# Performance work log

Measured on AMD Instinct MI355X. Metric: run time of the kernel, lower is better.

The kernel has to match this reference:

```python
import jax, jax.numpy as jnp
import numpy as np

B, N, D = 32, 2048, 16
PCD = 2        # point_cloud_dimensions
K_NN = 16      # k nearest neighbours
FILTERS = 64


def setup_inputs() -> dict:
    key = jax.random.key(0)
    k1, k2, k3 = jax.random.split(key, 3)
    x = jax.random.normal(k1, (B, N, D), dtype=jnp.float32)
    # 1x1 Conv2D == dense over the last (channel) dim: W [D, FILTERS], b [FILTERS]
    W = jax.random.normal(k2, (D, FILTERS), dtype=jnp.float32) * (1.0 / np.sqrt(D))
    b = jnp.zeros((FILTERS,), dtype=jnp.float32)
    return {"x": x, "W": W, "b": b}


def reference(x, W, b):
    # points = first PCD channels; features = full input (dynamic_coordinates=True)
    points = x[:, :, :PCD]                                   # [B,N,PCD]
    # squared pairwise distances: ||p_i||^2 + ||p_j||^2 - 2 p_i.p_j  -> [B,N,N]
    sq = jnp.sum(points * points, axis=-1)                   # [B,N]
    dist = sq[:, :, None] + sq[:, None, :] - 2.0 * jnp.einsum(
        'bnd,bmd->bnm', points, points)
    # k nearest neighbours (smallest distance) per point -> [B,N,k]
    _, idx = jax.lax.top_k(-dist, K_NN)
    # gather neighbour features: [B,N,k,D]
    neigh = jax.vmap(lambda f, i: f[i])(x, idx)
    centre = x[:, :, None, :]                                # [B,N,1,D]
    # NOTE: source concatenates along the neighbour axis -> [B,N,k+1,D]
    edges = jnp.concatenate([centre, neigh - centre], axis=2)
    # 1x1 conv (linear activation) over channel dim: [B,N,k+1,FILTERS]
    conv = jnp.einsum('bnkd,df->bnkf', edges, W) + b
    # Max pooling over neighbour axis: [B,N,FILTERS]
    pooled = jnp.max(conv, axis=2)
    # shortcut_input_features=True: concat original features
    return jnp.concatenate([pooled, x], axis=-1)             # [B,N,FILTERS+D]
```

## Files before the change

kernel.cpp:

```cpp
#include <hip/hip_runtime.h>


#define B_  32
#define N_  2048
#define D_  16
#define F_  64
#define K_  16
#define OUTD (F_ + D_)
#define NQ  64
#define NS  4
#define SPLIT (N_ / NS)

__global__ __launch_bounds__(256) void proj_kernel(const float* __restrict__ x,
                                                   const float* __restrict__ W,
                                                   float* __restrict__ Y) {
    __shared__ float Ws[D_ * F_];
    __shared__ float xs[16][D_];
    const int t = threadIdx.x;
    for (int i = t; i < D_ * F_; i += 256) Ws[i] = W[i];
    const int p0 = blockIdx.x * 16;
    ((float*)xs)[t] = x[(size_t)p0 * D_ + t];
    __syncthreads();
    const int w = t >> 6, f = t & 63;
#pragma unroll
    for (int i = 0; i < 4; i++) {
        const int pw = w * 4 + i;
        float acc = 0.f;
#pragma unroll
        for (int d = 0; d < D_; d++) acc = fmaf(xs[pw][d], Ws[d * F_ + f], acc);
        Y[(size_t)(p0 + pw) * F_ + f] = acc;
    }
}

__global__ __launch_bounds__(256, 4) void knn_kernel(const float* __restrict__ x,
                                                     const float* __restrict__ bias,
                                                     const float* __restrict__ Y,
                                                     float* __restrict__ out) {
    __shared__ float2 pts[N_];
    __shared__ float  sqs[N_];
    __shared__ float  arr_raw[NS - 1][NQ * 17];
    __shared__ float  Tq[NQ];
    __shared__ int    cnt[NQ];
    __shared__ int    tiecnt[NS][NQ];
    unsigned short (*tiebuf)[NQ][K_] =
        (unsigned short (*)[NQ][K_])&arr_raw[0][0];
    int (*idxL)[K_] = (int (*)[K_])((char*)&arr_raw[0][0] + 8192);

    const int b = blockIdx.x >> 5;
    const int qbase = (blockIdx.x & 31) * NQ;
    const int t = threadIdx.x;
    const int s = t >> 6;
    const int qi = t & 63;
    const int q = qbase + qi;

    const float* xb = x + (size_t)b * N_ * D_;
    for (int m = t; m < N_; m += 256) {
        float2 p = make_float2(xb[m * D_ + 0], xb[m * D_ + 1]);
        pts[m] = p;
        sqs[m] = __fadd_rn(__fmul_rn(p.x, p.x), __fmul_rn(p.y, p.y));
    }
    if (t < NQ) cnt[t] = 0;
    __syncthreads();

    const float2 qp = pts[q];
    const float sqn = sqs[q];

    float key[K_];
#pragma unroll
    for (int j = 0; j < K_; j++) key[j] = INFINITY;

    const int m0 = s * SPLIT, m1 = m0 + SPLIT;
#pragma unroll 4
    for (int m = m0; m < m1; m += 2) {
        float2 pa = pts[m];     float sa = sqs[m];
        float2 pb = pts[m + 1]; float sb = sqs[m + 1];
        float dota = __fmaf_rn(qp.y, pa.y, __fmul_rn(qp.x, pa.x));
        float da   = __fsub_rn(__fadd_rn(sqn, sa), __fmul_rn(2.f, dota));
        float dotb = __fmaf_rn(qp.y, pb.y, __fmul_rn(qp.x, pb.x));
        float db   = __fsub_rn(__fadd_rn(sqn, sb), __fmul_rn(2.f, dotb));
        float y0 = fminf(da, db), y1 = fmaxf(da, db);
#pragma unroll
        for (int j = K_ - 1; j >= 2; j--)
            key[j] = fminf(fminf(key[j], fmaxf(key[j - 1], y0)),
                           fmaxf(key[j - 2], y1));
        key[1] = fminf(fminf(key[1], fmaxf(key[0], y0)), y1);
        key[0] = fminf(key[0], y0);
    }

    if (s > 0) {
#pragma unroll
        for (int j = 0; j < K_; j++) arr_raw[s - 1][qi * 17 + j] = key[j];
    }
    __syncthreads();

    if (s == 0) {
        for (int ss = 0; ss < NS - 1; ss++) {
#pragma unroll
            for (int j = 0; j < K_; j += 2) {
                float y0 = arr_raw[ss][qi * 17 + j];
                float y1 = arr_raw[ss][qi * 17 + j + 1];
#pragma unroll
                for (int jj = K_ - 1; jj >= 2; jj--)
                    key[jj] = fminf(fminf(key[jj], fmaxf(key[jj - 1], y0)),
                                    fmaxf(key[jj - 2], y1));
                key[1] = fminf(fminf(key[1], fmaxf(key[0], y0)), y1);
                key[0] = fminf(key[0], y0);
            }
        }
        Tq[qi] = key[K_ - 1];
    }
    __syncthreads();

    const float T = Tq[qi];
    int tc = 0;
#pragma unroll 2
    for (int m = m0; m < m1; m++) {
        float2 p = pts[m];
        float dot = __fmaf_rn(qp.y, p.y, __fmul_rn(qp.x, p.x));
        float d   = __fsub_rn(__fadd_rn(sqn, sqs[m]), __fmul_rn(2.f, dot));
        if (d < T) {
            int slot = atomicAdd(&cnt[qi], 1);
            idxL[qi][slot] = m;
        } else if (d == T) {
            if (tc < K_) tiebuf[s][qi][tc] = (unsigned short)m;
            tc++;
        }
    }
    tiecnt[s][qi] = (tc < K_) ? tc : K_;
    __syncthreads();

    if (s == 0) {
        int c1 = cnt[qi];
        int w = c1;
        int need = K_ - c1;
        for (int ss = 0; ss < NS && need > 0; ss++) {
            int nn = tiecnt[ss][qi];
            for (int j = 0; j < nn && need > 0; j++) {
                idxL[qi][w++] = (int)tiebuf[ss][qi][j];
                need--;
            }
        }
    }
    __syncthreads();

    const int f = qi;
    const float bf = bias[f];
    const float* Yb = Y + (size_t)b * N_ * F_;
    for (int i = 0; i < 16; i++) {
        const int qq = s * 16 + i;
        const int gq = qbase + qq;
        const float yn = Yb[(size_t)gq * F_ + f];
        float M = -INFINITY;
#pragma unroll
        for (int k = 0; k < K_; k++) {
            int m = idxL[qq][k];
            M = fmaxf(M, Yb[(size_t)m * F_ + f]);
        }
        const size_t pb = (size_t)b * N_ + gq;
        out[pb * OUTD + f] = fmaxf(yn, M - yn) + bf;
        if (f < D_) out[pb * OUTD + F_ + f] = xb[(size_t)gq * D_ + f];
    }
}

extern "C" void kernel_launch(void* const* d_in, const int* in_sizes, int n_in,
                              void* d_out, int out_size, void* d_ws, size_t ws_size,
                              hipStream_t stream) {
    const float* x    = (const float*)d_in[0];
    const float* W    = (const float*)d_in[1];
    const float* bias = (const float*)d_in[2];
    float* out = (float*)d_out;

    float* Y = (float*)d_ws;

    proj_kernel<<<B_ * N_ / 16, 256, 0, stream>>>(x, W, Y);
    knn_kernel <<<B_ * (N_ / NQ), 256, 0, stream>>>(x, bias, Y, out);
}
```

Measured before the change: 259.4 us.

## Sort points by x and prune kNN scans with early termination

Adds a per-batch bitonic sort of points by their x coordinate, then has each query scan outward in both directions along the sorted order. A scan stops once the squared x-gap exceeds the current k-th distance plus a margin. This replaces the brute-force scan over all N points with a small local window. Tie handling is reworked to keep original-index order, so results should match the reference. The cost is an extra sort kernel with many block-level syncs, divergent per-thread loop lengths, and lower occupancy because of the added shared arrays.

Result: slower. 481.0 us (+85.5%).

```diff
diff --git a/kernel.cpp b/kernel.cpp
--- a/kernel.cpp
+++ b/kernel.cpp
@@ -9,17 +9,56 @@
 #define OUTD (F_ + D_)
 #define NQ  64
 #define NS  4
-#define SPLIT (N_ / NS)
+#define MARGIN 1e-3f
+
+__global__ __launch_bounds__(256) void sort_kernel(const float* __restrict__ x,
+                                                   float* __restrict__ xs,
+                                                   float* __restrict__ ys,
+                                                   unsigned short* __restrict__ oidx) {
+    __shared__ float keyL[N_];
+    __shared__ int   valL[N_];
+    const int bidx = blockIdx.x;
+    const int t = threadIdx.x;
+    const float* xb = x + (size_t)bidx * N_ * D_;
+    for (int m = t; m < N_; m += 256) { keyL[m] = xb[(size_t)m * D_]; valL[m] = m; }
+    for (int k = 2; k <= N_; k <<= 1) {
+        for (int j = k >> 1; j > 0; j >>= 1) {
+            __syncthreads();
+            for (int i = t; i < N_; i += 256) {
+                int ixj = i ^ j;
+                if (ixj > i) {
+                    float a = keyL[i], c = keyL[ixj];
+                    bool up = ((i & k) == 0);
+                    bool sw = up ? (a > c) : (a < c);
+                    if (sw) {
+                        keyL[i] = c; keyL[ixj] = a;
+                        int tv = valL[i]; valL[i] = valL[ixj]; valL[ixj] = tv;
+                    }
+                }
+            }
+        }
+    }
+    __syncthreads();
+    float* xso = xs + (size_t)bidx * N_;
+    float* yso = ys + (size_t)bidx * N_;
+    unsigned short* oio = oidx + (size_t)bidx * N_;
+    for (int p = t; p < N_; p += 256) {
+        int v = valL[p];
+        xso[p] = keyL[p];
+        yso[p] = xb[(size_t)v * D_ + 1];
+        oio[p] = (unsigned short)v;
+    }
+}
 
 __global__ __launch_bounds__(256) void proj_kernel(const float* __restrict__ x,
                                                    const float* __restrict__ W,
                                                    float* __restrict__ Y) {
     __shared__ float Ws[D_ * F_];
-    __shared__ float xs[16][D_];
+    __shared__ float xsh[16][D_];
     const int t = threadIdx.x;
     for (int i = t; i < D_ * F_; i += 256) Ws[i] = W[i];
     const int p0 = blockIdx.x * 16;
-    ((float*)xs)[t] = x[(size_t)p0 * D_ + t];
+    ((float*)xsh)[t] = x[(size_t)p0 * D_ + t];
     __syncthreads();
     const int w = t >> 6, f = t & 63;
 #pragma unroll
@@ -27,17 +66,22 @@
         const int pw = w * 4 + i;
         float acc = 0.f;
 #pragma unroll
-        for (int d = 0; d < D_; d++) acc = fmaf(xs[pw][d], Ws[d * F_ + f], acc);
+        for (int d = 0; d < D_; d++) acc = fmaf(xsh[pw][d], Ws[d * F_ + f], acc);
         Y[(size_t)(p0 + pw) * F_ + f] = acc;
     }
 }
 
-__global__ __launch_bounds__(256, 4) void knn_kernel(const float* __restrict__ x,
+__global__ __launch_bounds__(256, 3) void knn_kernel(const float* __restrict__ x,
                                                      const float* __restrict__ bias,
                                                      const float* __restrict__ Y,
+                                                     const float* __restrict__ xs,
+                                                     const float* __restrict__ ys,
+                                                     const unsigned short* __restrict__ oidx,
                                                      float* __restrict__ out) {
-    __shared__ float2 pts[N_];
-    __shared__ float  sqs[N_];
+    __shared__ float  xsL[N_];
+    __shared__ float  ysL[N_];
+    __shared__ float  sqL[N_];
+    __shared__ unsigned short oiL[N_];
     __shared__ float  arr_raw[NS - 1][NQ * 17];
     __shared__ float  Tq[NQ];
     __shared__ int    cnt[NQ];
@@ -53,31 +97,44 @@
     const int qi = t & 63;
     const int q = qbase + qi;
 
-    const float* xb = x + (size_t)b * N_ * D_;
+    const float* xsb = xs + (size_t)b * N_;
+    const float* ysb = ys + (size_t)b * N_;
+    const unsigned short* oib = oidx + (size_t)b * N_;
     for (int m = t; m < N_; m += 256) {
-        float2 p = make_float2(xb[m * D_ + 0], xb[m * D_ + 1]);
-        pts[m] = p;
-        sqs[m] = __fadd_rn(__fmul_rn(p.x, p.x), __fmul_rn(p.y, p.y));
+        float xv = xsb[m];
+        float yv = ysb[m];
+        xsL[m] = xv;
+        ysL[m] = yv;
+        sqL[m] = __fadd_rn(__fmul_rn(xv, xv), __fmul_rn(yv, yv));
+        oiL[m] = oib[m];
     }
     if (t < NQ) cnt[t] = 0;
     __syncthreads();
 
-    const float2 qp = pts[q];
-    const float sqn = sqs[q];
+    const float qx = xsL[q];
+    const float qy = ysL[q];
+    const float sqn = sqL[q];
+
+    const int pstart = q + ((s == 0) ? 0 : (s == 1) ? 1 : (s == 2) ? -1 : -2);
+    const int pstep  = (s < 2) ? 2 : -2;
 
     float key[K_];
 #pragma unroll
     for (int j = 0; j < K_; j++) key[j] = INFINITY;
 
-    const int m0 = s * SPLIT, m1 = m0 + SPLIT;
-#pragma unroll 4
-    for (int m = m0; m < m1; m += 2) {
-        float2 pa = pts[m];     float sa = sqs[m];
-        float2 pb = pts[m + 1]; float sb = sqs[m + 1];
-        float dota = __fmaf_rn(qp.y, pa.y, __fmul_rn(qp.x, pa.x));
-        float da   = __fsub_rn(__fadd_rn(sqn, sa), __fmul_rn(2.f, dota));
-        float dotb = __fmaf_rn(qp.y, pb.y, __fmul_rn(qp.x, pb.x));
-        float db   = __fsub_rn(__fadd_rn(sqn, sb), __fmul_rn(2.f, dotb));
+    for (int p = pstart; (unsigned)p < (unsigned)N_; p += 2 * pstep) {
+        float xma = xsL[p];
+        float dxa = xma - qx;
+        if (dxa * dxa > key[K_ - 1] + MARGIN) break;
+        float dota = __fmaf_rn(qy, ysL[p], __fmul_rn(qx, xma));
+        float da   = __fsub_rn(__fadd_rn(sqn, sqL[p]), __fmul_rn(2.f, dota));
+        float db = INFINITY;
+        const int p2 = p + pstep;
+        if ((unsigned)p2 < (unsigned)N_) {
+            float xmb = xsL[p2];
+            float dotb = __fmaf_rn(qy, ysL[p2], __fmul_rn(qx, xmb));
+            db = __fsub_rn(__fadd_rn(sqn, sqL[p2]), __fmul_rn(2.f, dotb));
+        }
         float y0 = fminf(da, db), y1 = fmaxf(da, db);
 #pragma unroll
         for (int j = K_ - 1; j >= 2; j--)
@@ -113,16 +170,23 @@
 
     const float T = Tq[qi];
     int tc = 0;
-#pragma unroll 2
-    for (int m = m0; m < m1; m++) {
-        float2 p = pts[m];
-        float dot = __fmaf_rn(qp.y, p.y, __fmul_rn(qp.x, p.x));
-        float d   = __fsub_rn(__fadd_rn(sqn, sqs[m]), __fmul_rn(2.f, dot));
+    for (int p = pstart; (unsigned)p < (unsigned)N_; p += pstep) {
+        float xm = xsL[p];
+        float dx = xm - qx;
+        if (dx * dx > T + MARGIN) break;
+        float dot = __fmaf_rn(qy, ysL[p], __fmul_rn(qx, xm));
+        float d   = __fsub_rn(__fadd_rn(sqn, sqL[p]), __fmul_rn(2.f, dot));
         if (d < T) {
             int slot = atomicAdd(&cnt[qi], 1);
-            idxL[qi][slot] = m;
+            idxL[qi][slot] = (int)oiL[p];
         } else if (d == T) {
-            if (tc < K_) tiebuf[s][qi][tc] = (unsigned short)m;
+            int oi = (int)oiL[p];
+            int pos = (tc < K_) ? tc : K_;
+            while (pos > 0 && (int)tiebuf[s][qi][pos - 1] > oi) {
+                if (pos < K_) tiebuf[s][qi][pos] = tiebuf[s][qi][pos - 1];
+                pos--;
+            }
+            if (pos < K_) tiebuf[s][qi][pos] = (unsigned short)oi;
             tc++;
         }
     }
@@ -131,14 +195,22 @@
 
     if (s == 0) {
         int c1 = cnt[qi];
-        int w = c1;
-        int need = K_ - c1;
-        for (int ss = 0; ss < NS && need > 0; ss++) {
-            int nn = tiecnt[ss][qi];
-            for (int j = 0; j < nn && need > 0; j++) {
-                idxL[qi][w++] = (int)tiebuf[ss][qi][j];
-                need--;
-            }
+        int l0 = tiecnt[0][qi], l1 = tiecnt[1][qi];
+        int l2 = tiecnt[2][qi], l3 = tiecnt[3][qi];
+        int p0 = 0, p1 = 0, p2 = 0, p3 = 0;
+        for (int w = c1; w < K_; w++) {
+            int v0 = (p0 < l0) ? (int)tiebuf[0][qi][p0] : 0x7fffffff;
+            int v1 = (p1 < l1) ? (int)tiebuf[1][qi][p1] : 0x7fffffff;
+            int v2 = (p2 < l2) ? (int)tiebuf[2][qi][p2] : 0x7fffffff;
+            int v3 = (p3 < l3) ? (int)tiebuf[3][qi][p3] : 0x7fffffff;
+            int m01 = (v0 <= v1) ? v0 : v1;
+            int m23 = (v2 <= v3) ? v2 : v3;
+            int mv  = (m01 <= m23) ? m01 : m23;
+            idxL[qi][w] = mv;
+            if (mv == v0) p0++;
+            else if (mv == v1) p1++;
+            else if (mv == v2) p2++;
+            else p3++;
         }
     }
     __syncthreads();
@@ -146,19 +218,20 @@
     const int f = qi;
     const float bf = bias[f];
     const float* Yb = Y + (size_t)b * N_ * F_;
+    const float* xb = x + (size_t)b * N_ * D_;
     for (int i = 0; i < 16; i++) {
         const int qq = s * 16 + i;
-        const int gq = qbase + qq;
-        const float yn = Yb[(size_t)gq * F_ + f];
+        const int oq = (int)oiL[qbase + qq];
+        const float yn = Yb[(size_t)oq * F_ + f];
         float M = -INFINITY;
 #pragma unroll
         for (int k = 0; k < K_; k++) {
             int m = idxL[qq][k];
             M = fmaxf(M, Yb[(size_t)m * F_ + f]);
         }
-        const size_t pb = (size_t)b * N_ + gq;
+        const size_t pb = (size_t)b * N_ + oq;
         out[pb * OUTD + f] = fmaxf(yn, M - yn) + bf;
-        if (f < D_) out[pb * OUTD + F_ + f] = xb[(size_t)gq * D_ + f];
+        if (f < D_) out[pb * OUTD + F_ + f] = xb[(size_t)oq * D_ + f];
     }
 }
 
@@ -170,8 +243,13 @@
     const float* bias = (const float*)d_in[2];
     float* out = (float*)d_out;
 
-    float* Y = (float*)d_ws;
-
+    char* ws = (char*)d_ws;
+    float* Y             = (float*)ws;
+    float* xs            = (float*)(ws + 16777216);
+    float* ys            = (float*)(ws + 16777216 + 262144);
+    unsigned short* oidx = (unsigned short*)(ws + 16777216 + 2*262144);
+
+    sort_kernel<<<B_, 256, 0, stream>>>(x, xs, ys, oidx);
     proj_kernel<<<B_ * N_ / 16, 256, 0, stream>>>(x, W, Y);
-    knn_kernel <<<B_ * (N_ / NQ), 256, 0, stream>>>(x, bias, Y, out);
-}
+    knn_kernel <<<B_ * (N_ / NQ), 256, 0, stream>>>(x, bias, Y, xs, ys, oidx, out);
+}
```
